# Performance work log

Hardware: AMD Instinct MI355X
Metric: run time of the kernel (lower is better)

Reference implementation:

```python
import jax, jax.numpy as jnp
import numpy as np

LN_EPS = 1e-5

def _layer_norm(x, g, b):
    m = jnp.mean(x, axis=-1, keepdims=True)
    v = jnp.mean((x - m) ** 2, axis=-1, keepdims=True)
    return (x - m) / jnp.sqrt(v + LN_EPS) * g + b

def setup_inputs() -> dict:
    key = jax.random.key(0)
    ks = jax.random.split(key, 16)
    B, L, D = 4, 2048, 1024
    DF = 4 * D
    s_in = 1.0 / np.sqrt(D)
    s_ff = 1.0 / np.sqrt(DF)
    # torch init of phazor: exp(2j*pi*arange(D)/D) * |randn|
    ang = 2.0 * np.pi * jnp.arange(D, dtype=jnp.float32) / D
    mag = jnp.abs(jax.random.normal(ks[0], (D,), jnp.float32))
    return {
        "x": jax.random.normal(ks[1], (B, L, D), jnp.float32),
        "hidden_real": jax.random.normal(ks[2], (B, D), jnp.float32),
        "hidden_imag": jax.random.normal(ks[3], (B, D), jnp.float32),
        "phazor_real": mag * jnp.cos(ang),
        "phazor_imag": mag * jnp.sin(ang),
        "phazor_init_real": jax.random.normal(ks[4], (D,), jnp.float32),
        "phazor_init_imag": jax.random.normal(ks[5], (D,), jnp.float32),
        "ln_gamma": jnp.ones((D,), jnp.float32),
        "ln_beta": jnp.zeros((D,), jnp.float32),
        "fc_w": jax.random.uniform(ks[6], (D, D), jnp.float32, -s_in, s_in),
        "fc_b": jax.random.uniform(ks[7], (D,), jnp.float32, -s_in, s_in),
        "w1": jax.random.uniform(ks[8], (DF, D), jnp.float32, -s_in, s_in),
        "b1": jax.random.uniform(ks[9], (DF,), jnp.float32, -s_in, s_in),
        "w2": jax.random.uniform(ks[10], (D, DF), jnp.float32, -s_ff, s_ff),
        "b2": jax.random.uniform(ks[11], (D,), jnp.float32, -s_ff, s_ff),
    }

def _spiral_conv(x, hidden, phazor_p, phazor_init):
    # x: [B,L,D] real, hidden: [B,D] complex
    B, L, D = x.shape
    amag = jnp.abs(phazor_p)
    phazor = phazor_p / amag * jnp.exp(-amag)                      # [D]
    prog = jnp.power(phazor[None, :], jnp.arange(L)[:, None])      # [L,D]
    filt = prog * phazor_init[None, :]                             # [L,D]
    filt_fft = jnp.fft.fft(filt, n=2 * L, axis=0)                  # [2L,D]
    x_fft = jnp.fft.fft(x.astype(jnp.complex64), n=2 * L, axis=1)  # [B,2L,D]
    conv = jnp.fft.ifft(filt_fft[None] * x_fft, axis=1)[:, :L]     # [B,L,D]
    conv_with_past = conv + jax.lax.stop_gradient(hidden)[:, None, :] * prog[None] * phazor[None, None]
    return conv_with_past.real, conv_with_past

def reference(x, hidden_real, hidden_imag, phazor_real, phazor_imag,
              phazor_init_real, phazor_init_imag, ln_gamma, ln_beta,
              fc_w, fc_b, w1, b1, w2, b2):
    hidden = hidden_real + 1j * hidden_imag
    phazor_p = phazor_real + 1j * phazor_imag
    phazor_init = phazor_init_real + 1j * phazor_init_imag

    x_res = x
    xn = _layer_norm(x, ln_gamma, ln_beta)
    s, new_hidden = _spiral_conv(xn, hidden, phazor_p, phazor_init)
    y = jax.nn.silu(jnp.einsum('bld,ed->ble', x, fc_w) + fc_b)
    h = s * y + x_res                      # dropout is identity (p=0 / eval)
    hn = _layer_norm(h, ln_gamma, ln_beta) # same LayerNorm instance reused
    ffn = jnp.einsum('blf,df->bld', jax.nn.silu(jnp.einsum('bld,fd->blf', hn, w1) + b1), w2) + b2
    out = ffn + h
    return out, new_hidden
```

## Files before the change

kernel.cpp:

```cpp
#include <hip/hip_runtime.h>

typedef unsigned short u16;
typedef unsigned int u32;
typedef float f32x4 __attribute__((ext_vector_type(4)));
typedef __bf16 bf16x8 __attribute__((ext_vector_type(8)));
typedef unsigned short u16x4 __attribute__((ext_vector_type(4)));

__device__ __forceinline__ float b2f(u16 u) {
    return __uint_as_float(((u32)u) << 16);
}
__device__ __forceinline__ u16 f2b(float f) {
    u32 u = __float_as_uint(f);
    return (u16)((u + 0x7FFFu + ((u >> 16) & 1u)) >> 16);
}
__device__ __forceinline__ bool is_f32(const u32* flag) {
    return flag[0] == 0x3F800000u;
}
__device__ __forceinline__ float lda(const void* p, size_t i, bool f) {
    return f ? ((const float*)p)[i] : b2f(((const u16*)p)[i]);
}
__device__ __forceinline__ void cmul(float& xr, float& xi, float yr, float yi) {
    float tr = xr * yr - xi * yi;
    xi = xr * yi + xi * yr;
    xr = tr;
}
__device__ __forceinline__ void gl2lds16(const void* g, void* l) {
    __builtin_amdgcn_global_load_lds(
        (const __attribute__((address_space(1))) void*)g,
        (__attribute__((address_space(3))) void*)l, 16, 0, 0);
}
__device__ __forceinline__ void wg_barrier() {
    asm volatile("" ::: "memory");
    __builtin_amdgcn_sched_barrier(0);
    __builtin_amdgcn_s_barrier();
    __builtin_amdgcn_sched_barrier(0);
    asm volatile("" ::: "memory");
}
#define VWAIT0 { asm volatile("s_waitcnt vmcnt(0)" ::: "memory"); __builtin_amdgcn_sched_barrier(0); }
#define VWAIT2 { asm volatile("s_waitcnt vmcnt(2)" ::: "memory"); __builtin_amdgcn_sched_barrier(0); }
#define VWAIT4 { asm volatile("s_waitcnt vmcnt(4)" ::: "memory"); __builtin_amdgcn_sched_barrier(0); }
#define LGKM0  { asm volatile("s_waitcnt lgkmcnt(0)" ::: "memory"); __builtin_amdgcn_sched_barrier(0); }

struct CvtArgs {
    const void* src[8];
    u16* dst[8];
    int n2[8];
    int tot;
};
__global__ __launch_bounds__(256) void cvtm_k(CvtArgs a, const u32* __restrict__ flag) {
    bool f = is_f32(flag);
    int i = blockIdx.x * 256 + threadIdx.x;
    if (i >= a.tot) return;
    int s = 0, base = 0;
    while (i - base >= a.n2[s]) { base += a.n2[s]; s++; }
    int k = i - base;
    if (f) {
        float2 v = ((const float2*)a.src[s])[k];
        ((u32*)a.dst[s])[k] = (u32)f2b(v.x) | ((u32)f2b(v.y) << 16);
    } else {
        ((u32*)a.dst[s])[k] = ((const u32*)a.src[s])[k];
    }
}

__global__ __launch_bounds__(256) void cvtln_k(const void* __restrict__ x,
                                               const u16* __restrict__ g,
                                               const u16* __restrict__ be,
                                               u16* __restrict__ xb,
                                               u16* __restrict__ xn, int D,
                                               const u32* __restrict__ flag) {
    bool f = is_f32(flag);
    int row = blockIdx.x;
    int tid = threadIdx.x;
    u16* xbr = xb + (size_t)row * D;
    float s = 0.f, s2 = 0.f;
    if (f) {
        const float* xr = (const float*)x + (size_t)row * D;
        for (int i = tid * 4; i < D; i += 1024) {
            float4 v = *(const float4*)&xr[i];
            u16x4 o;
            o.x = f2b(v.x); o.y = f2b(v.y); o.z = f2b(v.z); o.w = f2b(v.w);
            *(u16x4*)&xbr[i] = o;
            s  += (v.x + v.y) + (v.z + v.w);
            s2 += (v.x * v.x + v.y * v.y) + (v.z * v.z + v.w * v.w);
        }
    } else {
        const u16* xr = (const u16*)x + (size_t)row * D;
        for (int i = tid * 4; i < D; i += 1024) {
            u16x4 v = *(const u16x4*)&xr[i];
            *(u16x4*)&xbr[i] = v;
            float a0 = b2f(v.x), a1 = b2f(v.y), a2 = b2f(v.z), a3 = b2f(v.w);
            s  += (a0 + a1) + (a2 + a3);
            s2 += (a0 * a0 + a1 * a1) + (a2 * a2 + a3 * a3);
        }
    }
    for (int off = 32; off > 0; off >>= 1) {
        s  += __shfl_down(s,  off, 64);
        s2 += __shfl_down(s2, off, 64);
    }
    __shared__ float red[8];
    int wave = tid >> 6;
    if ((tid & 63) == 0) { red[wave * 2] = s; red[wave * 2 + 1] = s2; }
    __syncthreads();
    if (tid == 0) {
        float ts = 0.f, ts2 = 0.f;
        for (int w = 0; w < 4; w++) { ts += red[w * 2]; ts2 += red[w * 2 + 1]; }
        float m = ts / D;
        float v = ts2 / D - m * m;
        red[0] = m;
        red[1] = rsqrtf(v + 1e-5f);
    }
    __syncthreads();
    float m = red[0], inv = red[1];
    u16* xnr = xn + (size_t)row * D;
    for (int i = tid * 4; i < D; i += 1024) {
        u16x4 v = *(const u16x4*)&xbr[i];
        u16x4 gv = *(const u16x4*)&g[i];
        u16x4 bv = *(const u16x4*)&be[i];
        u16x4 r;
        r.x = f2b((b2f(v.x) - m) * inv * b2f(gv.x) + b2f(bv.x));
        r.y = f2b((b2f(v.y) - m) * inv * b2f(gv.y) + b2f(bv.y));
        r.z = f2b((b2f(v.z) - m) * inv * b2f(gv.z) + b2f(bv.z));
        r.w = f2b((b2f(v.w) - m) * inv * b2f(gv.w) + b2f(bv.w));
        *(u16x4*)&xnr[i] = r;
    }
}

__global__ __launch_bounds__(256) void ln_k(const u16* __restrict__ x,
                                            const u16* __restrict__ g,
                                            const u16* __restrict__ be,
                                            u16* __restrict__ o, int D) {
    int row = blockIdx.x;
    const u16* xr = x + (size_t)row * D;
    int tid = threadIdx.x;
    float s = 0.f, s2 = 0.f;
    for (int i = tid * 4; i < D; i += 1024) {
        u16x4 v = *(const u16x4*)&xr[i];
        float a0 = b2f(v.x), a1 = b2f(v.y), a2 = b2f(v.z), a3 = b2f(v.w);
        s  += (a0 + a1) + (a2 + a3);
        s2 += (a0 * a0 + a1 * a1) + (a2 * a2 + a3 * a3);
    }
    for (int off = 32; off > 0; off >>= 1) {
        s  += __shfl_down(s,  off, 64);
        s2 += __shfl_down(s2, off, 64);
    }
    __shared__ float red[8];
    int wave = tid >> 6;
    if ((tid & 63) == 0) { red[wave * 2] = s; red[wave * 2 + 1] = s2; }
    __syncthreads();
    if (tid == 0) {
        float ts = 0.f, ts2 = 0.f;
        for (int w = 0; w < 4; w++) { ts += red[w * 2]; ts2 += red[w * 2 + 1]; }
        float m = ts / D;
        float v = ts2 / D - m * m;
        red[0] = m;
        red[1] = rsqrtf(v + 1e-5f);
    }
    __syncthreads();
    float m = red[0], inv = red[1];
    u16* orow = o + (size_t)row * D;
    for (int i = tid * 4; i < D; i += 1024) {
        u16x4 v = *(const u16x4*)&xr[i];
        u16x4 gv = *(const u16x4*)&g[i];
        u16x4 bv = *(const u16x4*)&be[i];
        u16x4 r;
        r.x = f2b((b2f(v.x) - m) * inv * b2f(gv.x) + b2f(bv.x));
        r.y = f2b((b2f(v.y) - m) * inv * b2f(gv.y) + b2f(bv.y));
        r.z = f2b((b2f(v.z) - m) * inv * b2f(gv.z) + b2f(bv.z));
        r.w = f2b((b2f(v.w) - m) * inv * b2f(gv.w) + b2f(bv.w));
        *(u16x4*)&orow[i] = r;
    }
}

__global__ __launch_bounds__(256) void scan_partial_k(const u16* __restrict__ xn,
                                                      const void* __restrict__ phr_,
                                                      const void* __restrict__ phi_,
                                                      float2* __restrict__ T,
                                                      int L, int D, int C, int Kc,
                                                      const u32* __restrict__ flag) {
    bool f = is_f32(flag);
    int tid = blockIdx.x * 256 + threadIdx.x;
    int d = tid % D;
    int c = (tid / D) % C;
    int b = tid / (D * C);
    float pr = lda(phr_, d, f), pi = lda(phi_, d, f);
    float amag = fmaxf(sqrtf(pr * pr + pi * pi), 1e-12f);
    float sc = __expf(-amag) / amag;
    float phr = pr * sc, phi = pi * sc;
    float Tr = 0.f, Ti = 0.f;
    const u16* xp = xn + ((size_t)b * L + (size_t)c * Kc) * D + d;
    for (int t = 0; t < Kc; t++) {
        float x = b2f(xp[(size_t)t * D]);
        float nr = phr * Tr - phi * Ti + x;
        Ti = phr * Ti + phi * Tr;
        Tr = nr;
    }
    T[tid] = make_float2(Tr, Ti);
}

__global__ __launch_bounds__(256) void scan_prefix_k(const void* __restrict__ phr_,
                                                     const void* __restrict__ phi_,
                                                     const float2* __restrict__ T,
                                                     float2* __restrict__ E,
                                                     int D, int C, int Kc,
                                                     const u32* __restrict__ flag) {
    bool f = is_f32(flag);
    int tid = blockIdx.x * 256 + threadIdx.x;
    int d = tid % D;
    int b = tid / D;
    float pr = lda(phr_, d, f), pi = lda(phi_, d, f);
    float amag = fmaxf(sqrtf(pr * pr + pi * pi), 1e-12f);
    float sc = __expf(-amag) / amag;
    float phr = pr * sc, phi = pi * sc;
    float kr = phr, ki = phi;
    for (int s = 1; s < Kc; s <<= 1) cmul(kr, ki, kr, ki);
    float cr = 0.f, ci = 0.f;
    for (int c = 0; c < C; c++) {
        size_t i = ((size_t)b * C + c) * D + d;
        E[i] = make_float2(cr, ci);
        float2 t = T[i];
        cmul(cr, ci, kr, ki);
        cr += t.x; ci += t.y;
    }
}

__global__ __launch_bounds__(256) void scan_final_k(const u16* __restrict__ xn,
                                                    const void* __restrict__ phr_,
                                                    const void* __restrict__ phi_,
                                                    const void* __restrict__ pir_,
                                                    const void* __restrict__ pii_,
                                                    const void* __restrict__ hr_,
                                                    const void* __restrict__ hi_,
                                                    const float2* __restrict__ E,
                                                    u16* __restrict__ sws,
                                                    void* __restrict__ dout,
                                                    int MD, int out_elems,
                                                    int L, int D, int C, int Kc,
                                                    const u32* __restrict__ flag) {
    bool f = is_f32(flag);
    int tid = blockIdx.x * 256 + threadIdx.x;
    int d = tid % D;
    int c = (tid / D) % C;
    int b = tid / (D * C);
    float pr = lda(phr_, d, f), pi = lda(phi_, d, f);
    float amag = fmaxf(sqrtf(pr * pr + pi * pi), 1e-12f);
    float sc = __expf(-amag) / amag;
    float phr = pr * sc, phi = pi * sc;
    float kr = phr, ki = phi;
    for (int s = 1; s < Kc; s <<= 1) cmul(kr, ki, kr, ki);
    float Pr = phr, Pi = phi;
    for (int j = 0; j < c; j++) cmul(Pr, Pi, kr, ki);
    float ir = lda(pir_, d, f), ii = lda(pii_, d, f);
    float hr = lda(hr_, (size_t)b * D + d, f), hi = lda(hi_, (size_t)b * D + d, f);
    float2 e = E[tid];
    float Sr = e.x, Si = e.y;
    const bool full = (out_elems >= 3 * MD);
    size_t mbase = (size_t)b * L + (size_t)c * Kc;
    for (int t = 0; t < Kc; t++) {
        size_t off = (mbase + t) * D + d;
        float x = b2f(xn[off]);
        float nr = phr * Sr - phi * Si + x;
        Si = phr * Si + phi * Sr;
        Sr = nr;
        float cr = ir * Sr - ii * Si + hr * Pr - hi * Pi;
        float ci = ir * Si + ii * Sr + hr * Pi + hi * Pr;
        sws[off] = f2b(cr);
        if (f) {
            float* fo = (float*)dout;
            if (full) {
                *(float2*)&fo[(size_t)MD + 2 * off] = make_float2(cr, ci);
            } else {
                fo[(size_t)MD + off] = cr;
            }
        } else {
            u16* uo = (u16*)dout;
            if (full) {
                *(u32*)&uo[(size_t)MD + 2 * off] =
                    (u32)f2b(cr) | ((u32)f2b(ci) << 16);
            } else {
                uo[(size_t)MD + off] = f2b(cr);
            }
        }
        cmul(Pr, Pi, phr, phi);
    }
}

template <int MODE>
__global__ __launch_bounds__(256) void gemm128(const u16* __restrict__ A,
                                               const u16* __restrict__ Bm,
                                               int M, int N, int K,
                                               const u16* __restrict__ bias,
                                               const u16* __restrict__ sbuf,
                                               const u16* __restrict__ xbuf,
                                               u16* __restrict__ out,
                                               void* __restrict__ outv,
                                               const u32* __restrict__ flag) {
    __shared__ u16 As[2][128 * 64];
    __shared__ u16 Bs[2][128 * 64];
    const int tid = threadIdx.x;
    const int wave = tid >> 6, lane = tid & 63;
    const int quad = lane >> 4, l16 = lane & 15;

    const int NT = N >> 7;
    const int j = blockIdx.x;
    const int gsize = 8 * NT;
    const int mg  = j / gsize;
    const int rem = j - mg * gsize;
    const int nt  = rem >> 3;
    const int mi  = rem & 7;
    const int bm = (mg * 8 + mi) * 128, bn = nt * 128;

    const int wrow = (wave >> 1) * 64, wcol = (wave & 1) * 64;

    f32x4 acc[4][4] = {};

    const int lr = lane >> 3;
    const int sl = (lane & 7) ^ lr;
    const size_t goff = (size_t)lr * K + sl * 8;
    const size_t K8 = (size_t)K * 8;
    const u16* aG = A  + (size_t)(bm + wave * 32) * K + goff;
    const u16* bG = Bm + (size_t)(bn + wave * 32) * K + goff;

#define STG8(B_, t_) { \
        const u16* ga = aG + (size_t)(t_) * 64; \
        const u16* gb = bG + (size_t)(t_) * 64; \
        gl2lds16(ga,          &As[B_][(wave * 32) * 64]); \
        gl2lds16(ga + K8,     &As[B_][(wave * 32 + 8) * 64]); \
        gl2lds16(ga + 2 * K8, &As[B_][(wave * 32 + 16) * 64]); \
        gl2lds16(ga + 3 * K8, &As[B_][(wave * 32 + 24) * 64]); \
        gl2lds16(gb,          &Bs[B_][(wave * 32) * 64]); \
        gl2lds16(gb + K8,     &Bs[B_][(wave * 32 + 8) * 64]); \
        gl2lds16(gb + 2 * K8, &Bs[B_][(wave * 32 + 16) * 64]); \
        gl2lds16(gb + 3 * K8, &Bs[B_][(wave * 32 + 24) * 64]); }

#define RD_A(B_, m_, ks_) (*(const bf16x8*)&As[B_][(wrow + (m_) * 16 + l16) * 64 + \
        ((((ks_) * 4 + quad) ^ (l16 & 7)) << 3)])
#define RD_B(B_, n_, ks_) (*(const bf16x8*)&Bs[B_][(wcol + (n_) * 16 + l16) * 64 + \
        ((((ks_) * 4 + quad) ^ (l16 & 7)) << 3)])

#define FMK(mm, nn, ks) acc[mm][nn] = __builtin_amdgcn_mfma_f32_16x16x32_bf16( \
        av[mm][ks], bv[nn][ks], acc[mm][nn], 0, 0, 0)

#define ITER128(CUR, t_) { \
        const bool stg = (t_) + 1 < KT; \
        if (stg) STG8(CUR ^ 1, (t_) + 1); \
        av[0][0] = RD_A(CUR, 0, 0); av[1][0] = RD_A(CUR, 1, 0); \
        av[2][0] = RD_A(CUR, 2, 0); av[3][0] = RD_A(CUR, 3, 0); \
        bv[0][0] = RD_B(CUR, 0, 0); bv[1][0] = RD_B(CUR, 1, 0); \
        bv[2][0] = RD_B(CUR, 2, 0); bv[3][0] = RD_B(CUR, 3, 0); \
        av[0][1] = RD_A(CUR, 0, 1); av[1][1] = RD_A(CUR, 1, 1); \
        av[2][1] = RD_A(CUR, 2, 1); av[3][1] = RD_A(CUR, 3, 1); \
        bv[0][1] = RD_B(CUR, 0, 1); bv[1][1] = RD_B(CUR, 1, 1); \
        bv[2][1] = RD_B(CUR, 2, 1); bv[3][1] = RD_B(CUR, 3, 1); \
        FMK(0, 0, 0); FMK(0, 1, 0); FMK(1, 0, 0); FMK(1, 1, 0); \
        FMK(0, 2, 0); FMK(0, 3, 0); FMK(1, 2, 0); FMK(1, 3, 0); \
        FMK(2, 0, 0); FMK(2, 1, 0); FMK(3, 0, 0); FMK(3, 1, 0); \
        FMK(2, 2, 0); FMK(2, 3, 0); FMK(3, 2, 0); FMK(3, 3, 0); \
        FMK(0, 0, 1); FMK(0, 1, 1); FMK(1, 0, 1); FMK(1, 1, 1); \
        FMK(0, 2, 1); FMK(0, 3, 1); FMK(1, 2, 1); FMK(1, 3, 1); \
        FMK(2, 0, 1); FMK(2, 1, 1); FMK(3, 0, 1); FMK(3, 1, 1); \
        FMK(2, 2, 1); FMK(2, 3, 1); FMK(3, 2, 1); FMK(3, 3, 1); \
        if (stg) { VWAIT0 } \
        wg_barrier(); }

    bf16x8 av[4][2], bv[4][2];
    const int KT = K >> 6;

    STG8(0, 0);
    VWAIT0; wg_barrier();

    for (int t = 0; t < KT; t += 2) {
        ITER128(0, t);
        ITER128(1, t + 1);
    }

    bool f = (MODE == 2) ? is_f32(flag) : false;
#pragma unroll
    for (int m = 0; m < 4; m++) {
#pragma unroll
        for (int n = 0; n < 4; n++) {
            int colg = bn + wcol + n * 16 + l16;
            float bsv = b2f(bias[colg]);
#pragma unroll
            for (int r = 0; r < 4; r++) {
                int rowg = bm + wrow + m * 16 + quad * 4 + r;
                size_t idx = (size_t)rowg * N + colg;
                float v = acc[m][n][r] + bsv;
                if (MODE == 0) {
                    float y = v / (1.f + __expf(-v));
                    float hv = b2f(sbuf[idx]) * y + b2f(xbuf[idx]);
                    out[idx] = f2b(hv);
                } else if (MODE == 1) {
                    float y = v / (1.f + __expf(-v));
                    out[idx] = f2b(y);
                } else {
                    float o = v + b2f(xbuf[idx]);
                    if (f) ((float*)outv)[idx] = o;
                    else   ((u16*)outv)[idx] = f2b(o);
                }
            }
        }
    }
#undef STG8
#undef RD_A
#undef RD_B
#undef FMK
#undef ITER128
}

template <int MODE, int BN>
__global__ __launch_bounds__(512) void gemm_nt(const u16* __restrict__ A,
                                               const u16* __restrict__ Bm,
                                               int M, int N, int K,
                                               const u16* __restrict__ bias,
                                               const u16* __restrict__ sbuf,
                                               const u16* __restrict__ xbuf,
                                               u16* __restrict__ out,
                                               void* __restrict__ outv,
                                               const u32* __restrict__ flag) {
    __shared__ u16 As[2][256 * 64];
    __shared__ u16 Bs[2][BN * 64];
    const int tid = threadIdx.x;
    const int wave = tid >> 6, lane = tid & 63;
    const int quad = lane >> 4, l16 = lane & 15;

    const int NT = N / BN;
    const int j = blockIdx.x;
    const int gsize = 8 * NT;
    const int mg  = j / gsize;
    const int rem = j - mg * gsize;
    const int nt  = rem >> 3;
    const int mi  = rem & 7;
    const int bm = (mg * 8 + mi) * 256, bn = nt * BN;

    const int wrow = (wave >> 2) * 128, wcol = (wave & 3) * 64;

    f32x4 acc[8][4] = {};

    const int lr = lane >> 3;
    const int sl = (lane & 7) ^ lr;
    const size_t goff = (size_t)lr * K + sl * 8;
    const size_t K8 = (size_t)K * 8;
    const u16* aG = A  + (size_t)(bm + wave * 16) * K + goff;
    const u16* bG = Bm + (size_t)(bn + wave * 16) * K + goff;

#define STG_A(B_, t_, h_) { \
        const u16* ga = aG + (size_t)(t_) * 64 + (size_t)(h_) * 128 * K; \
        gl2lds16(ga,      &As[B_][((h_) * 128 + wave * 16) * 64]); \
        gl2lds16(ga + K8, &As[B_][((h_) * 128 + wave * 16 + 8) * 64]); }
#define STG_B(B_, t_, h_) { \
        const u16* gb = bG + (size_t)(t_) * 64 + (size_t)(h_) * 128 * K; \
        gl2lds16(gb,      &Bs[B_][((h_) * 128 + wave * 16) * 64]); \
        gl2lds16(gb + K8, &Bs[B_][((h_) * 128 + wave * 16 + 8) * 64]); }

#define RDA(B_, m_, ks_) (*(const bf16x8*)&As[B_][(wrow + (m_) * 16 + l16) * 64 + \
        ((((ks_) * 4 + quad) ^ (l16 & 7)) << 3)])
#define RDB(B_, n_, ks_) (*(const bf16x8*)&Bs[B_][(wcol + (n_) * 16 + l16) * 64 + \
        ((((ks_) * 4 + quad) ^ (l16 & 7)) << 3)])

#define LDA4(RB, mh) { \
        av[0][0] = RDA(RB, (mh) * 4 + 0, 0); av[0][1] = RDA(RB, (mh) * 4 + 0, 1); \
        av[1][0] = RDA(RB, (mh) * 4 + 1, 0); av[1][1] = RDA(RB, (mh) * 4 + 1, 1); \
        av[2][0] = RDA(RB, (mh) * 4 + 2, 0); av[2][1] = RDA(RB, (mh) * 4 + 2, 1); \
        av[3][0] = RDA(RB, (mh) * 4 + 3, 0); av[3][1] = RDA(RB, (mh) * 4 + 3, 1); }
#define LDB2(RB, nh) { \
        bv[(nh) * 2 + 0][0] = RDB(RB, (nh) * 2 + 0, 0); \
        bv[(nh) * 2 + 0][1] = RDB(RB, (nh) * 2 + 0, 1); \
        bv[(nh) * 2 + 1][0] = RDB(RB, (nh) * 2 + 1, 0); \
        bv[(nh) * 2 + 1][1] = RDB(RB, (nh) * 2 + 1, 1); }

#define FM(mi_, ni_, ks_) acc[mi_][ni_] = __builtin_amdgcn_mfma_f32_16x16x32_bf16( \
        av[(mi_) & 3][ks_], bv[ni_][ks_], acc[mi_][ni_], 0, 0, 0)
#define MFMA16(mh, nh) { \
        __builtin_amdgcn_s_setprio(1); \
        FM((mh)*4+0, (nh)*2+0, 0); FM((mh)*4+0, (nh)*2+1, 0); \
        FM((mh)*4+1, (nh)*2+0, 0); FM((mh)*4+1, (nh)*2+1, 0); \
        FM((mh)*4+2, (nh)*2+0, 0); FM((mh)*4+2, (nh)*2+1, 0); \
        FM((mh)*4+3, (nh)*2+0, 0); FM((mh)*4+3, (nh)*2+1, 0); \
        FM((mh)*4+0, (nh)*2+0, 1); FM((mh)*4+0, (nh)*2+1, 1); \
        FM((mh)*4+1, (nh)*2+0, 1); FM((mh)*4+1, (nh)*2+1, 1); \
        FM((mh)*4+2, (nh)*2+0, 1); FM((mh)*4+2, (nh)*2+1, 1); \
        FM((mh)*4+3, (nh)*2+0, 1); FM((mh)*4+3, (nh)*2+1, 1); \
        __builtin_amdgcn_s_setprio(0); }

    bf16x8 av[4][2], bv[4][2];
    const int KT = K >> 6;

    STG_A(0, 0, 0); STG_B(0, 0, 0); STG_B(0, 0, 1); STG_A(0, 0, 1);
    VWAIT4; wg_barrier();
#define TILE256(RB, SB, t_) { \
        const bool stg = (t_) + 1 < KT; \
         \
        LDA4(RB, 0); LDB2(RB, 0); \
        if (stg) STG_A(SB, (t_) + 1, 0);       \
        wg_barrier(); LGKM0; \
        MFMA16(0, 0); \
        if (stg) { VWAIT4 } else { VWAIT2 }    \
        wg_barrier(); \
         \
        LDB2(RB, 1); \
        if (stg) STG_B(SB, (t_) + 1, 0);       \
        wg_barrier(); LGKM0; \
        MFMA16(0, 1); \
        if (stg) { VWAIT4 } else { VWAIT0 }    \
        wg_barrier(); \
         \
        LDA4(RB, 1); \
        if (stg) STG_B(SB, (t_) + 1, 1);       \
        wg_barrier(); LGKM0; \
        MFMA16(1, 0); \
        wg_barrier(); \
         \
        if (stg) STG_A(SB, (t_) + 1, 1);       \
        wg_barrier(); LGKM0; \
        MFMA16(1, 1); \
        if (stg) { VWAIT4 }                    \
        wg_barrier(); }
    for (int t = 0; t < KT; t += 2) {
        TILE256(0, 1, t);
        TILE256(1, 0, t + 1);
    }
#undef TILE256

    bool f = (MODE == 2) ? is_f32(flag) : false;
#pragma unroll
    for (int m = 0; m < 8; m++) {
#pragma unroll
        for (int n = 0; n < 4; n++) {
            int colg = bn + wcol + n * 16 + l16;
            float bsv = b2f(bias[colg]);
#pragma unroll
            for (int r = 0; r < 4; r++) {
                int rowg = bm + wrow + m * 16 + quad * 4 + r;
                size_t idx = (size_t)rowg * N + colg;
                float v = acc[m][n][r] + bsv;
                if (MODE == 0) {
                    float y = v / (1.f + __expf(-v));
                    float hv = b2f(sbuf[idx]) * y + b2f(xbuf[idx]);
                    out[idx] = f2b(hv);
                } else if (MODE == 1) {
                    float y = v / (1.f + __expf(-v));
                    out[idx] = f2b(y);
                } else {
                    float o = v + b2f(xbuf[idx]);
                    if (f) ((float*)outv)[idx] = o;
                    else   ((u16*)outv)[idx] = f2b(o);
                }
            }
        }
    }
#undef STG_A
#undef STG_B
#undef RDA
#undef RDB
#undef LDA4
#undef LDB2
#undef FM
#undef MFMA16
}

extern "C" void kernel_launch(void* const* d_in, const int* in_sizes, int n_in,
                              void* d_out, int out_size, void* d_ws, size_t ws_size,
                              hipStream_t stream) {
    const void* x   = d_in[0];
    const void* hr  = d_in[1];
    const void* hi  = d_in[2];
    const void* phr = d_in[3];
    const void* phi = d_in[4];
    const void* pir = d_in[5];
    const void* pii = d_in[6];
    const void* g   = d_in[7];
    const void* be  = d_in[8];
    const void* fcw = d_in[9];
    const void* fcb = d_in[10];
    const void* w1  = d_in[11];
    const void* b1  = d_in[12];
    const void* w2  = d_in[13];
    const void* b2  = d_in[14];
    const u32* flag = (const u32*)g;

    const int D  = in_sizes[3];
    const int Bb = in_sizes[1] / D;
    const int L  = in_sizes[0] / (Bb * D);
    const int DF = in_sizes[12];
    const int M  = Bb * L;
    const int Kc = 32, C = L / Kc;
    const int MD = M * D;

    char* ws = (char*)d_ws;
    size_t MD2 = (size_t)MD * 2;
    u16*    xb  = (u16*)(ws);
    u16*    xn  = (u16*)(ws + MD2);
    u16*    sws = (u16*)(ws + 2 * MD2);
    float2* T   = (float2*)(ws + 3 * MD2);
    float2* E   = (float2*)(ws + 3 * MD2 + (size_t)Bb * C * D * 8);
    u16*    a1  = (u16*)(ws);
    u16*    h   = (u16*)(ws + 4 * MD2);
    u16*    hn  = (u16*)(ws + 5 * MD2);
    char*   wp  = ws + 6 * MD2;
    u16* fcwb = (u16*)wp; wp += (size_t)D * D * 2;
    u16* w1b  = (u16*)wp; wp += (size_t)DF * D * 2;
    u16* w2b  = (u16*)wp; wp += (size_t)D * DF * 2;
    u16* fcbb = (u16*)wp; wp += (size_t)D * 2;
    u16* b1b  = (u16*)wp; wp += (size_t)DF * 2;
    u16* b2b  = (u16*)wp; wp += (size_t)D * 2;
    u16* gb   = (u16*)wp; wp += (size_t)D * 2;
    u16* bb   = (u16*)wp; wp += (size_t)D * 2;

    CvtArgs ca;
    const void* srcs[8] = { fcw, w1, w2, fcb, b1, b2, g, be };
    u16* dsts[8] = { fcwb, w1b, w2b, fcbb, b1b, b2b, gb, bb };
    size_t ns[8] = { (size_t)D * D, (size_t)DF * D, (size_t)D * DF,
                     (size_t)D, (size_t)DF, (size_t)D, (size_t)D, (size_t)D };
    int tot = 0;
    for (int i = 0; i < 8; i++) {
        ca.src[i] = srcs[i];
        ca.dst[i] = dsts[i];
        ca.n2[i] = (int)(ns[i] / 2);
        tot += ca.n2[i];
    }
    ca.tot = tot;
    cvtm_k<<<(tot + 255) / 256, 256, 0, stream>>>(ca, flag);

    cvtln_k<<<M, 256, 0, stream>>>(x, gb, bb, xb, xn, D, flag);
    scan_partial_k<<<(Bb * C * D) / 256, 256, 0, stream>>>(xn, phr, phi, T, L, D, C, Kc, flag);
    scan_prefix_k<<<(Bb * D) / 256, 256, 0, stream>>>(phr, phi, T, E, D, C, Kc, flag);
    scan_final_k<<<(Bb * C * D) / 256, 256, 0, stream>>>(xn, phr, phi, pir, pii, hr, hi,
                                                         E, sws, d_out, MD, out_size,
                                                         L, D, C, Kc, flag);
    gemm128<0><<<(M / 128) * (D / 128), 256, 0, stream>>>(xb, fcwb, M, D, D, fcbb, sws, xb, h, nullptr, flag);
    ln_k<<<M, 256, 0, stream>>>(h, gb, bb, hn, D);
    gemm_nt<1, 256><<<(M / 256) * (DF / 256), 512, 0, stream>>>(hn, w1b, M, DF, D, b1b, nullptr, nullptr, a1, nullptr, flag);
    gemm128<2><<<(M / 128) * (D / 128), 256, 0, stream>>>(a1, w2b, M, D, DF, b2b, nullptr, h, nullptr, d_out, flag);
}
```

Baseline: 402.1 us.

## Parallelize chunk prefix scan across wave lanes and use 8-wave gemm128 tiles

Adds a wave-level parallel prefix scan over the 64 chunk carries. Each lane holds one chunk and combines carries by shuffle with doubling powers of the decay factor, replacing the serial per-channel loop over chunks when C is 64. The 128x128 GEMM kernel now runs 512 threads as 8 waves, each computing a 64x32 sub-tile, to raise per-CU wave count and latency hiding. The risks are fewer MFMAs per LDS read per wave, extra shuffle math in the scan, and small numeric reordering of the complex accumulation.

```diff
diff --git a/kernel.cpp b/kernel.cpp
--- a/kernel.cpp
+++ b/kernel.cpp
@@ -221,6 +221,43 @@
         cmul(cr, ci, kr, ki);
         cr += t.x; ci += t.y;
     }
+}
+
+__global__ __launch_bounds__(256) void scan_prefix_wave_k(const void* __restrict__ phr_,
+                                                          const void* __restrict__ phi_,
+                                                          const float2* __restrict__ T,
+                                                          float2* __restrict__ E,
+                                                          int D, int Kc,
+                                                          const u32* __restrict__ flag) {
+    bool f = is_f32(flag);
+    int gtid = blockIdx.x * 256 + threadIdx.x;
+    int w = gtid >> 6;
+    int lane = gtid & 63;
+    int d = w % D;
+    int b = w / D;
+    float pr = lda(phr_, d, f), pi = lda(phi_, d, f);
+    float amag = fmaxf(sqrtf(pr * pr + pi * pi), 1e-12f);
+    float sc = __expf(-amag) / amag;
+    float phr = pr * sc, phi = pi * sc;
+    float kr = phr, ki = phi;
+    for (int s = 1; s < Kc; s <<= 1) cmul(kr, ki, kr, ki);
+    size_t i = ((size_t)b * 64 + lane) * D + d;
+    float2 t = T[i];
+    float sr = t.x, si = t.y;
+    float wr = kr, wi = ki;
+    for (int s = 1; s < 64; s <<= 1) {
+        float or_ = __shfl_up(sr, s, 64);
+        float oi_ = __shfl_up(si, s, 64);
+        if (lane >= s) {
+            sr += or_ * wr - oi_ * wi;
+            si += or_ * wi + oi_ * wr;
+        }
+        cmul(wr, wi, wr, wi);
+    }
+    float er = __shfl_up(sr, 1, 64);
+    float ei = __shfl_up(si, 1, 64);
+    if (lane == 0) { er = 0.f; ei = 0.f; }
+    E[i] = make_float2(er, ei);
 }
 
 __global__ __launch_bounds__(256) void scan_final_k(const u16* __restrict__ xn,
@@ -285,7 +322,7 @@
 }
 
 template <int MODE>
-__global__ __launch_bounds__(256) void gemm128(const u16* __restrict__ A,
+__global__ __launch_bounds__(512) void gemm128(const u16* __restrict__ A,
                                                const u16* __restrict__ Bm,
                                                int M, int N, int K,
                                                const u16* __restrict__ bias,
@@ -309,28 +346,24 @@
     const int mi  = rem & 7;
     const int bm = (mg * 8 + mi) * 128, bn = nt * 128;
 
-    const int wrow = (wave >> 1) * 64, wcol = (wave & 1) * 64;
-
-    f32x4 acc[4][4] = {};
+    const int wrow = (wave >> 2) * 64, wcol = (wave & 3) * 32;
+
+    f32x4 acc[4][2] = {};
 
     const int lr = lane >> 3;
     const int sl = (lane & 7) ^ lr;
     const size_t goff = (size_t)lr * K + sl * 8;
     const size_t K8 = (size_t)K * 8;
-    const u16* aG = A  + (size_t)(bm + wave * 32) * K + goff;
-    const u16* bG = Bm + (size_t)(bn + wave * 32) * K + goff;
-
-#define STG8(B_, t_) { \
+    const u16* aG = A  + (size_t)(bm + wave * 16) * K + goff;
+    const u16* bG = Bm + (size_t)(bn + wave * 16) * K + goff;
+
+#define STG4(B_, t_) { \
         const u16* ga = aG + (size_t)(t_) * 64; \
         const u16* gb = bG + (size_t)(t_) * 64; \
-        gl2lds16(ga,          &As[B_][(wave * 32) * 64]); \
-        gl2lds16(ga + K8,     &As[B_][(wave * 32 + 8) * 64]); \
-        gl2lds16(ga + 2 * K8, &As[B_][(wave * 32 + 16) * 64]); \
-        gl2lds16(ga + 3 * K8, &As[B_][(wave * 32 + 24) * 64]); \
-        gl2lds16(gb,          &Bs[B_][(wave * 32) * 64]); \
-        gl2lds16(gb + K8,     &Bs[B_][(wave * 32 + 8) * 64]); \
-        gl2lds16(gb + 2 * K8, &Bs[B_][(wave * 32 + 16) * 64]); \
-        gl2lds16(gb + 3 * K8, &Bs[B_][(wave * 32 + 24) * 64]); }
+        gl2lds16(ga,      &As[B_][(wave * 16) * 64]); \
+        gl2lds16(ga + K8, &As[B_][(wave * 16 + 8) * 64]); \
+        gl2lds16(gb,      &Bs[B_][(wave * 16) * 64]); \
+        gl2lds16(gb + K8, &Bs[B_][(wave * 16 + 8) * 64]); }
 
 #define RD_A(B_, m_, ks_) (*(const bf16x8*)&As[B_][(wrow + (m_) * 16 + l16) * 64 + \
         ((((ks_) * 4 + quad) ^ (l16 & 7)) << 3)])
@@ -342,30 +375,24 @@
 
 #define ITER128(CUR, t_) { \
         const bool stg = (t_) + 1 < KT; \
-        if (stg) STG8(CUR ^ 1, (t_) + 1); \
+        if (stg) STG4(CUR ^ 1, (t_) + 1); \
         av[0][0] = RD_A(CUR, 0, 0); av[1][0] = RD_A(CUR, 1, 0); \
         av[2][0] = RD_A(CUR, 2, 0); av[3][0] = RD_A(CUR, 3, 0); \
         bv[0][0] = RD_B(CUR, 0, 0); bv[1][0] = RD_B(CUR, 1, 0); \
-        bv[2][0] = RD_B(CUR, 2, 0); bv[3][0] = RD_B(CUR, 3, 0); \
         av[0][1] = RD_A(CUR, 0, 1); av[1][1] = RD_A(CUR, 1, 1); \
         av[2][1] = RD_A(CUR, 2, 1); av[3][1] = RD_A(CUR, 3, 1); \
         bv[0][1] = RD_B(CUR, 0, 1); bv[1][1] = RD_B(CUR, 1, 1); \
-        bv[2][1] = RD_B(CUR, 2, 1); bv[3][1] = RD_B(CUR, 3, 1); \
         FMK(0, 0, 0); FMK(0, 1, 0); FMK(1, 0, 0); FMK(1, 1, 0); \
-        FMK(0, 2, 0); FMK(0, 3, 0); FMK(1, 2, 0); FMK(1, 3, 0); \
         FMK(2, 0, 0); FMK(2, 1, 0); FMK(3, 0, 0); FMK(3, 1, 0); \
-        FMK(2, 2, 0); FMK(2, 3, 0); FMK(3, 2, 0); FMK(3, 3, 0); \
         FMK(0, 0, 1); FMK(0, 1, 1); FMK(1, 0, 1); FMK(1, 1, 1); \
-        FMK(0, 2, 1); FMK(0, 3, 1); FMK(1, 2, 1); FMK(1, 3, 1); \
         FMK(2, 0, 1); FMK(2, 1, 1); FMK(3, 0, 1); FMK(3, 1, 1); \
-        FMK(2, 2, 1); FMK(2, 3, 1); FMK(3, 2, 1); FMK(3, 3, 1); \
         if (stg) { VWAIT0 } \
         wg_barrier(); }
 
-    bf16x8 av[4][2], bv[4][2];
+    bf16x8 av[4][2], bv[2][2];
     const int KT = K >> 6;
 
-    STG8(0, 0);
+    STG4(0, 0);
     VWAIT0; wg_barrier();
 
     for (int t = 0; t < KT; t += 2) {
@@ -377,7 +404,7 @@
 #pragma unroll
     for (int m = 0; m < 4; m++) {
 #pragma unroll
-        for (int n = 0; n < 4; n++) {
+        for (int n = 0; n < 2; n++) {
             int colg = bn + wcol + n * 16 + l16;
             float bsv = b2f(bias[colg]);
 #pragma unroll
@@ -400,7 +427,7 @@
             }
         }
     }
-#undef STG8
+#undef STG4
 #undef RD_A
 #undef RD_B
 #undef FMK
@@ -623,12 +650,16 @@
 
     cvtln_k<<<M, 256, 0, stream>>>(x, gb, bb, xb, xn, D, flag);
     scan_partial_k<<<(Bb * C * D) / 256, 256, 0, stream>>>(xn, phr, phi, T, L, D, C, Kc, flag);
-    scan_prefix_k<<<(Bb * D) / 256, 256, 0, stream>>>(phr, phi, T, E, D, C, Kc, flag);
+    if (C == 64) {
+        scan_prefix_wave_k<<<(Bb * D * 64) / 256, 256, 0, stream>>>(phr, phi, T, E, D, Kc, flag);
+    } else {
+        scan_prefix_k<<<(Bb * D) / 256, 256, 0, stream>>>(phr, phi, T, E, D, C, Kc, flag);
+    }
     scan_final_k<<<(Bb * C * D) / 256, 256, 0, stream>>>(xn, phr, phi, pir, pii, hr, hi,
                                                          E, sws, d_out, MD, out_size,
                                                          L, D, C, Kc, flag);
-    gemm128<0><<<(M / 128) * (D / 128), 256, 0, stream>>>(xb, fcwb, M, D, D, fcbb, sws, xb, h, nullptr, flag);
+    gemm128<0><<<(M / 128) * (D / 128), 512, 0, stream>>>(xb, fcwb, M, D, D, fcbb, sws, xb, h, nullptr, flag);
     ln_k<<<M, 256, 0, stream>>>(h, gb, bb, hn, D);
     gemm_nt<1, 256><<<(M / 256) * (DF / 256), 512, 0, stream>>>(hn, w1b, M, DF, D, b1b, nullptr, nullptr, a1, nullptr, flag);
-    gemm128<2><<<(M / 128) * (D / 128), 256, 0, stream>>>(a1, w2b, M, D, DF, b2b, nullptr, h, nullptr, d_out, flag);
-}
+    gemm128<2><<<(M / 128) * (D / 128), 512, 0, stream>>>(a1, w2b, M, D, DF, b2b, nullptr, h, nullptr, d_out, flag);
+}
```

Result: faster. 380.3 us (median of 2 runs) (-5.4%).
